# Optimization experiments

Measured on AMD Instinct MI355X. Metric: run time of the kernel, lower is better.

## Reference

```python
import jax, jax.numpy as jnp
import numpy as np

F_SIZE = 256
N_HEAD = 4
D_HEAD = F_SIZE // N_HEAD
B = 16384
E = 31  # number of 'other' entities


def setup_inputs() -> dict:
    key = jax.random.key(0)
    ks = jax.random.split(key, 9)
    s = 1.0 / np.sqrt(F_SIZE)  # ~ nn.Linear init scale
    inp = {
        "ego": jax.random.normal(ks[0], (B, 1, F_SIZE), dtype=jnp.float32),
        "others": jax.random.normal(ks[1], (B, E, F_SIZE), dtype=jnp.float32),
        "mask": jax.random.randint(ks[2], (B, E + 1), 0, 2).astype(bool),
        "Wq": jax.random.uniform(ks[3], (F_SIZE, F_SIZE), jnp.float32, -s, s),
        "Wk": jax.random.uniform(ks[4], (F_SIZE, F_SIZE), jnp.float32, -s, s),
        "Wv": jax.random.uniform(ks[5], (F_SIZE, F_SIZE), jnp.float32, -s, s),
        "Wok": jax.random.uniform(ks[6], (F_SIZE, F_SIZE), jnp.float32, -s, s),
        "Wov": jax.random.uniform(ks[7], (F_SIZE, F_SIZE), jnp.float32, -s, s),
        "Wc": jax.random.uniform(ks[8], (F_SIZE, F_SIZE), jnp.float32, -s, s),
    }
    return inp


def reference(ego, others, mask, Wq, Wk, Wv, Wok, Wov, Wc):
    b = others.shape[0]
    e = others.shape[1]
    # nn.Linear(bias=False): y = x @ W.T
    ego_q = (ego @ Wq.T).reshape(b, 1, N_HEAD, D_HEAD)
    ego_k = (ego @ Wk.T).reshape(b, 1, N_HEAD, D_HEAD)
    ego_v = (ego @ Wv.T).reshape(b, 1, N_HEAD, D_HEAD)
    oth_k = (others @ Wok.T).reshape(b, e, N_HEAD, D_HEAD)
    oth_v = (others @ Wov.T).reshape(b, e, N_HEAD, D_HEAD)
    all_k = jnp.concatenate([ego_k, oth_k], axis=1)  # (b, e+1, h, d)
    all_v = jnp.concatenate([ego_v, oth_v], axis=1)
    # scores: single query per head -> (b, h, 1, e+1)
    scores = jnp.einsum('bqhd,bkhd->bhqk', ego_q, all_k) / np.sqrt(D_HEAD)
    scores = jnp.where(mask[:, None, None, :], jnp.float32(-1e9), scores)
    attn = jax.nn.softmax(scores, axis=-1)
    value = jnp.einsum('bhqk,bkhd->bqhd', attn, all_v).reshape(b, F_SIZE)
    res = ((value @ Wc.T) + ego[:, 0, :]) * 0.5
    return res, attn
```

## Files before the change

### kernel.cpp

```cpp
#include <hip/hip_runtime.h>
#include <hip/hip_bf16.h>

typedef __attribute__((ext_vector_type(8))) short bf16x8;
typedef __attribute__((ext_vector_type(4))) float f32x4;

#define NB 16384
#define NE 31

static __device__ __forceinline__ unsigned short f2b(float f) {
  unsigned int u = __builtin_bit_cast(unsigned int, f);
  return (unsigned short)((u + 0x7fffu + ((u >> 16) & 1u)) >> 16);
}
static __device__ __forceinline__ float b2f(unsigned short h) {
  return __builtin_bit_cast(float, ((unsigned int)h) << 16);
}


__global__ void k0_base(const float* __restrict__ wq, const float* __restrict__ wk,
                        const float* __restrict__ wv, const float* __restrict__ wc,
                        unsigned short* __restrict__ W1, unsigned short* __restrict__ W2) {
  int r = blockIdx.x, k = threadIdx.x;
  if (r < 256) {
    W1[r * 256 + k] = f2b(0.125f * wq[r * 256 + k]);
  } else if (r < 512) {
    W1[r * 256 + k] = f2b(wk[(r - 256) * 256 + k]);
  } else if (r < 768) {
    W1[r * 256 + k] = f2b(wv[(r - 512) * 256 + k]);
  } else {
    int n = r - 768;
    W2[n * 1280 + 1024 + k] = f2b(wc[n * 256 + k]);
  }
}

__global__ void k0_wqo(const float* __restrict__ wq, const float* __restrict__ wok,
                       unsigned short* __restrict__ W1) {
  int m = blockIdx.x;
  int k = threadIdx.x;
  int h = m >> 8, c = m & 255;
  float acc = 0.f;
#pragma unroll 8
  for (int d = 0; d < 64; ++d)
    acc = fmaf(wq[(h * 64 + d) * 256 + k], wok[(h * 64 + d) * 256 + c], acc);
  W1[(768 + m) * 256 + k] = f2b(0.125f * acc);
}

__global__ void k0_g(const float* __restrict__ wov, const float* __restrict__ wc,
                     unsigned short* __restrict__ W2) {
  int n = blockIdx.x;
  int t = threadIdx.x;
#pragma unroll 1
  for (int mi = 0; mi < 4; ++mi) {
    float acc = 0.f;
#pragma unroll 8
    for (int d = 0; d < 64; ++d)
      acc = fmaf(wov[(mi * 64 + d) * 256 + t], wc[n * 256 + mi * 64 + d], acc);
    W2[n * 1280 + mi * 256 + t] = f2b(acc);
  }
}

__global__ __launch_bounds__(256, 2)
void k1b(const float* __restrict__ ego, const unsigned short* __restrict__ W1,
         unsigned short* __restrict__ qkv2) {
  __shared__ __align__(16) unsigned short Al[64 * 256];
  const int tid = threadIdx.x;
  const int bM = blockIdx.x * 64;
#pragma unroll
  for (int it = 0; it < 8; ++it) {
    int c = tid + it * 256;
    int row = c >> 5, k8 = c & 31;
    const float4* g = (const float4*)(ego + (size_t)(bM + row) * 256 + k8 * 8);
    float4 x = g[0], y = g[1];
    float t[8] = {x.x, x.y, x.z, x.w, y.x, y.y, y.z, y.w};
    bf16x8 v;
#pragma unroll
    for (int j = 0; j < 8; ++j) v[j] = (short)f2b(t[j]);
    int byteoff = row * 512 + ((k8 * 16) ^ ((row & 7) << 4));
    *(bf16x8*)((char*)Al + byteoff) = v;
  }
  __syncthreads();
  const int w = tid >> 6, lane = tid & 63, lr = lane & 15, lkg = lane >> 4;
#pragma unroll 1
  for (int cb = 0; cb < 7; ++cb) {
    int bN = w * 448 + cb * 64;
    f32x4 acc[4][4];
#pragma unroll
    for (int mt = 0; mt < 4; ++mt)
#pragma unroll
      for (int nt = 0; nt < 4; ++nt) acc[mt][nt] = (f32x4){0.f, 0.f, 0.f, 0.f};
#pragma unroll
    for (int kk = 0; kk < 8; ++kk) {
      int kidx = kk * 32 + lkg * 8;
      bf16x8 bfr[4];
#pragma unroll
      for (int nt = 0; nt < 4; ++nt)
        bfr[nt] = *(const bf16x8*)(W1 + (size_t)(bN + nt * 16 + lr) * 256 + kidx);
#pragma unroll
      for (int mt = 0; mt < 4; ++mt) {
        int row = mt * 16 + lr;
        int byteoff = row * 512 + ((kidx * 2) ^ ((row & 7) << 4));
        bf16x8 a = *(const bf16x8*)((const char*)Al + byteoff);
#pragma unroll
        for (int nt = 0; nt < 4; ++nt)
          acc[mt][nt] = __builtin_amdgcn_mfma_f32_16x16x32_bf16(a, bfr[nt], acc[mt][nt], 0, 0, 0);
      }
    }
#pragma unroll
    for (int mt = 0; mt < 4; ++mt)
#pragma unroll
      for (int nt = 0; nt < 4; ++nt)
#pragma unroll
        for (int j = 0; j < 4; ++j) {
          int row = bM + mt * 16 + lkg * 4 + j;
          int col = bN + nt * 16 + lr;
          qkv2[(size_t)row * 1792 + col] = f2b(acc[mt][nt][j]);
        }
  }
}

__global__ __launch_bounds__(256, 4)
void ks_attn(const float* __restrict__ others, const int* __restrict__ mask,
             const unsigned short* __restrict__ qkv2,
             unsigned short* __restrict__ u,
             float* __restrict__ attnout) {
  __shared__ __align__(16) unsigned short Xr[32 * 264];
  __shared__ __align__(16) unsigned short Qo_l[1024];
  __shared__ __align__(16) unsigned short qk_l[768];
  __shared__ float sco_l[4][32];
  __shared__ float Pl[4][32];
  const int tid = threadIdx.x;
  const size_t b = blockIdx.x;

  {
    int e = tid >> 3, c = tid & 7;
    if (e < 31) {
      const float4* src = (const float4*)(others) + ((b * 31 + e) * 64 + c * 8);
      float4 f[8];
#pragma unroll
      for (int j = 0; j < 8; ++j) f[j] = src[j];
#pragma unroll
      for (int j = 0; j < 4; ++j) {
        bf16x8 v;
        v[0] = (short)f2b(f[2 * j].x);     v[1] = (short)f2b(f[2 * j].y);
        v[2] = (short)f2b(f[2 * j].z);     v[3] = (short)f2b(f[2 * j].w);
        v[4] = (short)f2b(f[2 * j + 1].x); v[5] = (short)f2b(f[2 * j + 1].y);
        v[6] = (short)f2b(f[2 * j + 1].z); v[7] = (short)f2b(f[2 * j + 1].w);
        *(bf16x8*)(&Xr[e * 264 + c * 32 + j * 8]) = v;
      }
    } else {
      bf16x8 z = (bf16x8){0, 0, 0, 0, 0, 0, 0, 0};
#pragma unroll
      for (int j = 0; j < 4; ++j) *(bf16x8*)(&Xr[31 * 264 + c * 32 + j * 8]) = z;
    }
    if (tid < 224) {
      bf16x8 v = *(const bf16x8*)(qkv2 + b * 1792 + tid * 8);
      if (tid < 96) *(bf16x8*)(&qk_l[tid * 8]) = v;
      else          *(bf16x8*)(&Qo_l[(tid - 96) * 8]) = v;
    }
  }
  __syncthreads();

  const int w = tid >> 6, lane = tid & 63, lr = lane & 15, lkg = lane >> 4;

  if (w < 2) {
    f32x4 acc = (f32x4){0.f, 0.f, 0.f, 0.f};
#pragma unroll
    for (int kk = 0; kk < 8; ++kk) {
      bf16x8 a = *(const bf16x8*)(&Qo_l[(lr & 3) * 256 + kk * 32 + lkg * 8]);
      bf16x8 bb = *(const bf16x8*)(&Xr[(w * 16 + lr) * 264 + kk * 32 + lkg * 8]);
      acc = __builtin_amdgcn_mfma_f32_16x16x32_bf16(a, bb, acc, 0, 0, 0);
    }
    if (lkg == 0) {
      int n = w * 16 + lr;
      if (n < NE) {
#pragma unroll
        for (int j = 0; j < 4; ++j) sco_l[j][1 + n] = acc[j];
      }
    }
  } else if (w == 2) {
    int h = lane >> 4, i = lane & 15;
    const unsigned short* q4 = &qk_l[h * 64 + i * 4];
    const unsigned short* k4p = &qk_l[256 + h * 64 + i * 4];
    float s = 0.f;
#pragma unroll
    for (int j = 0; j < 4; ++j) s += b2f(q4[j]) * b2f(k4p[j]);
#pragma unroll
    for (int off = 1; off < 16; off <<= 1) s += __shfl_xor(s, off, 16);
    if (i == 0) sco_l[h][0] = s;
  }
  __syncthreads();

  {
    int key = lane & 31;
    float s = sco_l[w][key];
    if (mask[b * 32 + key] != 0) s = -1e9f;
    float mx = s;
#pragma unroll
    for (int off = 1; off < 32; off <<= 1) mx = fmaxf(mx, __shfl_xor(mx, off, 32));
    float ex = __expf(s - mx);
    float sm = ex;
#pragma unroll
    for (int off = 1; off < 32; off <<= 1) sm += __shfl_xor(sm, off, 32);
    float p = ex / sm;
    if (lane < 32) {
      Pl[w][key] = p;
      attnout[b * 128 + w * 32 + key] = p;
    }
  }

  {
    float a0 = 0.f, a1 = 0.f, a2 = 0.f, a3 = 0.f;
#pragma unroll
    for (int e = 0; e < NE; ++e) {
      float p = Pl[w][1 + e];
      ushort4 xv = *(const ushort4*)(&Xr[e * 264 + lane * 4]);
      a0 = fmaf(p, b2f(xv.x), a0);
      a1 = fmaf(p, b2f(xv.y), a1);
      a2 = fmaf(p, b2f(xv.z), a2);
      a3 = fmaf(p, b2f(xv.w), a3);
    }
    ushort4 st;
    st.x = f2b(a0); st.y = f2b(a1); st.z = f2b(a2); st.w = f2b(a3);
    *(ushort4*)(u + b * 1280 + w * 256 + lane * 4) = st;
    float p0 = Pl[w][0];
    u[b * 1280 + 1024 + w * 64 + lane] = f2b(p0 * b2f(qk_l[512 + w * 64 + lane]));
  }
}

__global__ __launch_bounds__(256, 2)
void k4_out(const unsigned short* __restrict__ u, const unsigned short* __restrict__ W2,
            const float* __restrict__ ego, float* __restrict__ out) {
  __shared__ __align__(16) unsigned short Au[32 * 256];
  const int tid = threadIdx.x;
  const int bM = blockIdx.x * 32;
  const int w = tid >> 6, lane = tid & 63, lr = lane & 15, lkg = lane >> 4;
  f32x4 acc[2][4];
#pragma unroll
  for (int mt = 0; mt < 2; ++mt)
#pragma unroll
    for (int nt = 0; nt < 4; ++nt) acc[mt][nt] = (f32x4){0.f, 0.f, 0.f, 0.f};
#pragma unroll 1
  for (int kc = 0; kc < 5; ++kc) {
#pragma unroll
    for (int it = 0; it < 4; ++it) {
      int c = tid + it * 256;
      int row = c >> 5, k8 = c & 31;
      bf16x8 v = *(const bf16x8*)(u + (size_t)(bM + row) * 1280 + kc * 256 + k8 * 8);
      int byteoff = row * 512 + ((k8 * 16) ^ ((row & 7) << 4));
      *(bf16x8*)((char*)Au + byteoff) = v;
    }
    __syncthreads();
#pragma unroll
    for (int kk = 0; kk < 8; ++kk) {
      int kidx = kk * 32 + lkg * 8;
      bf16x8 bfr[4];
#pragma unroll
      for (int nt = 0; nt < 4; ++nt)
        bfr[nt] = *(const bf16x8*)(W2 + (size_t)(w * 64 + nt * 16 + lr) * 1280 + kc * 256 + kidx);
#pragma unroll
      for (int mt = 0; mt < 2; ++mt) {
        int row = mt * 16 + lr;
        int byteoff = row * 512 + ((kidx * 2) ^ ((row & 7) << 4));
        bf16x8 a = *(const bf16x8*)((const char*)Au + byteoff);
#pragma unroll
        for (int nt = 0; nt < 4; ++nt)
          acc[mt][nt] = __builtin_amdgcn_mfma_f32_16x16x32_bf16(a, bfr[nt], acc[mt][nt], 0, 0, 0);
      }
    }
    __syncthreads();
  }
#pragma unroll
  for (int mt = 0; mt < 2; ++mt)
#pragma unroll
    for (int nt = 0; nt < 4; ++nt)
#pragma unroll
      for (int j = 0; j < 4; ++j) {
        int row = bM + mt * 16 + lkg * 4 + j;
        int col = w * 64 + nt * 16 + lr;
        out[(size_t)row * 256 + col] = (acc[mt][nt][j] + ego[(size_t)row * 256 + col]) * 0.5f;
      }
}

extern "C" void kernel_launch(void* const* d_in, const int* in_sizes, int n_in,
                              void* d_out, int out_size, void* d_ws, size_t ws_size,
                              hipStream_t stream) {
  const float* ego    = (const float*)d_in[0];
  const float* others = (const float*)d_in[1];
  const int*   mask   = (const int*)d_in[2];
  const float* wq  = (const float*)d_in[3];
  const float* wk  = (const float*)d_in[4];
  const float* wv  = (const float*)d_in[5];
  const float* wok = (const float*)d_in[6];
  const float* wov = (const float*)d_in[7];
  const float* wc  = (const float*)d_in[8];

  unsigned short* W1   = (unsigned short*)d_ws;
  unsigned short* W2   = W1 + 1792 * 256;
  unsigned short* qkv2 = W2 + 256 * 1280;
  unsigned short* u    = qkv2 + (size_t)NB * 1792;

  float* res  = (float*)d_out;
  float* attn = res + (size_t)NB * 256;

  hipLaunchKernelGGL(k0_base, dim3(1024), dim3(256), 0, stream, wq, wk, wv, wc, W1, W2);
  hipLaunchKernelGGL(k0_wqo,  dim3(1024), dim3(256), 0, stream, wq, wok, W1);
  hipLaunchKernelGGL(k0_g,    dim3(256),  dim3(256), 0, stream, wov, wc, W2);
  hipLaunchKernelGGL(k1b,     dim3(256),  dim3(256), 0, stream, ego, W1, qkv2);
  hipLaunchKernelGGL(ks_attn, dim3(NB),   dim3(256), 0, stream, others, mask, qkv2, u, attn);
  hipLaunchKernelGGL(k4_out,  dim3(512),  dim3(256), 0, stream, u, W2, ego, res);
}
```

Baseline: 268.1 us.

## Merge weight-prep kernels, halve k1b tile, swizzle Xr LDS, raise attn occupancy

```diff
diff --git a/kernel.cpp b/kernel.cpp
--- a/kernel.cpp
+++ b/kernel.cpp
@@ -15,57 +15,51 @@
   return __builtin_bit_cast(float, ((unsigned int)h) << 16);
 }
 
-
-__global__ void k0_base(const float* __restrict__ wq, const float* __restrict__ wk,
-                        const float* __restrict__ wv, const float* __restrict__ wc,
-                        unsigned short* __restrict__ W1, unsigned short* __restrict__ W2) {
+__global__ void k0_all(const float* __restrict__ wq, const float* __restrict__ wk,
+                       const float* __restrict__ wv, const float* __restrict__ wok,
+                       const float* __restrict__ wov, const float* __restrict__ wc,
+                       unsigned short* __restrict__ W1, unsigned short* __restrict__ W2) {
   int r = blockIdx.x, k = threadIdx.x;
-  if (r < 256) {
-    W1[r * 256 + k] = f2b(0.125f * wq[r * 256 + k]);
-  } else if (r < 512) {
-    W1[r * 256 + k] = f2b(wk[(r - 256) * 256 + k]);
-  } else if (r < 768) {
-    W1[r * 256 + k] = f2b(wv[(r - 512) * 256 + k]);
-  } else {
-    int n = r - 768;
-    W2[n * 1280 + 1024 + k] = f2b(wc[n * 256 + k]);
-  }
-}
-
-__global__ void k0_wqo(const float* __restrict__ wq, const float* __restrict__ wok,
-                       unsigned short* __restrict__ W1) {
-  int m = blockIdx.x;
-  int k = threadIdx.x;
-  int h = m >> 8, c = m & 255;
-  float acc = 0.f;
-#pragma unroll 8
-  for (int d = 0; d < 64; ++d)
-    acc = fmaf(wq[(h * 64 + d) * 256 + k], wok[(h * 64 + d) * 256 + c], acc);
-  W1[(768 + m) * 256 + k] = f2b(0.125f * acc);
-}
-
-__global__ void k0_g(const float* __restrict__ wov, const float* __restrict__ wc,
-                     unsigned short* __restrict__ W2) {
-  int n = blockIdx.x;
-  int t = threadIdx.x;
-#pragma unroll 1
-  for (int mi = 0; mi < 4; ++mi) {
+  if (r < 1024) {
+    if (r < 256) {
+      W1[r * 256 + k] = f2b(0.125f * wq[r * 256 + k]);
+    } else if (r < 512) {
+      W1[r * 256 + k] = f2b(wk[(r - 256) * 256 + k]);
+    } else if (r < 768) {
+      W1[r * 256 + k] = f2b(wv[(r - 512) * 256 + k]);
+    } else {
+      int n = r - 768;
+      W2[n * 1280 + 1024 + k] = f2b(wc[n * 256 + k]);
+    }
+  } else if (r < 2048) {
+    int m = r - 1024;
+    int h = m >> 8, c = m & 255;
     float acc = 0.f;
 #pragma unroll 8
     for (int d = 0; d < 64; ++d)
-      acc = fmaf(wov[(mi * 64 + d) * 256 + t], wc[n * 256 + mi * 64 + d], acc);
-    W2[n * 1280 + mi * 256 + t] = f2b(acc);
+      acc = fmaf(wq[(h * 64 + d) * 256 + k], wok[(h * 64 + d) * 256 + c], acc);
+    W1[(768 + m) * 256 + k] = f2b(0.125f * acc);
+  } else {
+    int n = r - 2048;
+#pragma unroll 1
+    for (int mi = 0; mi < 4; ++mi) {
+      float acc = 0.f;
+#pragma unroll 8
+      for (int d = 0; d < 64; ++d)
+        acc = fmaf(wov[(mi * 64 + d) * 256 + k], wc[n * 256 + mi * 64 + d], acc);
+      W2[n * 1280 + mi * 256 + k] = f2b(acc);
+    }
   }
 }
 
 __global__ __launch_bounds__(256, 2)
 void k1b(const float* __restrict__ ego, const unsigned short* __restrict__ W1,
          unsigned short* __restrict__ qkv2) {
-  __shared__ __align__(16) unsigned short Al[64 * 256];
+  __shared__ __align__(16) unsigned short Al[32 * 256];
   const int tid = threadIdx.x;
-  const int bM = blockIdx.x * 64;
-#pragma unroll
-  for (int it = 0; it < 8; ++it) {
+  const int bM = blockIdx.x * 32;
+#pragma unroll
+  for (int it = 0; it < 4; ++it) {
     int c = tid + it * 256;
     int row = c >> 5, k8 = c & 31;
     const float4* g = (const float4*)(ego + (size_t)(bM + row) * 256 + k8 * 8);
@@ -82,9 +76,9 @@
 #pragma unroll 1
   for (int cb = 0; cb < 7; ++cb) {
     int bN = w * 448 + cb * 64;
-    f32x4 acc[4][4];
-#pragma unroll
-    for (int mt = 0; mt < 4; ++mt)
+    f32x4 acc[2][4];
+#pragma unroll
+    for (int mt = 0; mt < 2; ++mt)
 #pragma unroll
       for (int nt = 0; nt < 4; ++nt) acc[mt][nt] = (f32x4){0.f, 0.f, 0.f, 0.f};
 #pragma unroll
@@ -95,7 +89,7 @@
       for (int nt = 0; nt < 4; ++nt)
         bfr[nt] = *(const bf16x8*)(W1 + (size_t)(bN + nt * 16 + lr) * 256 + kidx);
 #pragma unroll
-      for (int mt = 0; mt < 4; ++mt) {
+      for (int mt = 0; mt < 2; ++mt) {
         int row = mt * 16 + lr;
         int byteoff = row * 512 + ((kidx * 2) ^ ((row & 7) << 4));
         bf16x8 a = *(const bf16x8*)((const char*)Al + byteoff);
@@ -105,7 +99,7 @@
       }
     }
 #pragma unroll
-    for (int mt = 0; mt < 4; ++mt)
+    for (int mt = 0; mt < 2; ++mt)
 #pragma unroll
       for (int nt = 0; nt < 4; ++nt)
 #pragma unroll
@@ -117,12 +111,12 @@
   }
 }
 
-__global__ __launch_bounds__(256, 4)
+__global__ __launch_bounds__(256, 6)
 void ks_attn(const float* __restrict__ others, const int* __restrict__ mask,
              const unsigned short* __restrict__ qkv2,
              unsigned short* __restrict__ u,
              float* __restrict__ attnout) {
-  __shared__ __align__(16) unsigned short Xr[32 * 264];
+  __shared__ __align__(16) unsigned short Xr[32 * 256];
   __shared__ __align__(16) unsigned short Qo_l[1024];
   __shared__ __align__(16) unsigned short qk_l[768];
   __shared__ float sco_l[4][32];
@@ -134,22 +128,29 @@
     int e = tid >> 3, c = tid & 7;
     if (e < 31) {
       const float4* src = (const float4*)(others) + ((b * 31 + e) * 64 + c * 8);
-      float4 f[8];
-#pragma unroll
-      for (int j = 0; j < 8; ++j) f[j] = src[j];
-#pragma unroll
-      for (int j = 0; j < 4; ++j) {
-        bf16x8 v;
-        v[0] = (short)f2b(f[2 * j].x);     v[1] = (short)f2b(f[2 * j].y);
-        v[2] = (short)f2b(f[2 * j].z);     v[3] = (short)f2b(f[2 * j].w);
-        v[4] = (short)f2b(f[2 * j + 1].x); v[5] = (short)f2b(f[2 * j + 1].y);
-        v[6] = (short)f2b(f[2 * j + 1].z); v[7] = (short)f2b(f[2 * j + 1].w);
-        *(bf16x8*)(&Xr[e * 264 + c * 32 + j * 8]) = v;
+#pragma unroll
+      for (int h = 0; h < 2; ++h) {
+        float4 f[4];
+#pragma unroll
+        for (int j = 0; j < 4; ++j) f[j] = src[h * 4 + j];
+#pragma unroll
+        for (int j = 0; j < 2; ++j) {
+          bf16x8 v;
+          v[0] = (short)f2b(f[2 * j].x);     v[1] = (short)f2b(f[2 * j].y);
+          v[2] = (short)f2b(f[2 * j].z);     v[3] = (short)f2b(f[2 * j].w);
+          v[4] = (short)f2b(f[2 * j + 1].x); v[5] = (short)f2b(f[2 * j + 1].y);
+          v[6] = (short)f2b(f[2 * j + 1].z); v[7] = (short)f2b(f[2 * j + 1].w);
+          int byteoff = e * 512 + ((c * 64 + h * 32 + j * 16) ^ ((e & 7) << 4));
+          *(bf16x8*)((char*)Xr + byteoff) = v;
+        }
       }
     } else {
       bf16x8 z = (bf16x8){0, 0, 0, 0, 0, 0, 0, 0};
 #pragma unroll
-      for (int j = 0; j < 4; ++j) *(bf16x8*)(&Xr[31 * 264 + c * 32 + j * 8]) = z;
+      for (int q4 = 0; q4 < 4; ++q4) {
+        int byteoff = 31 * 512 + ((c * 64 + q4 * 16) ^ ((31 & 7) << 4));
+        *(bf16x8*)((char*)Xr + byteoff) = z;
+      }
     }
     if (tid < 224) {
       bf16x8 v = *(const bf16x8*)(qkv2 + b * 1792 + tid * 8);
@@ -166,7 +167,9 @@
 #pragma unroll
     for (int kk = 0; kk < 8; ++kk) {
       bf16x8 a = *(const bf16x8*)(&Qo_l[(lr & 3) * 256 + kk * 32 + lkg * 8]);
-      bf16x8 bb = *(const bf16x8*)(&Xr[(w * 16 + lr) * 264 + kk * 32 + lkg * 8]);
+      int row = w * 16 + lr;
+      int byteoff = row * 512 + ((kk * 64 + lkg * 16) ^ ((row & 7) << 4));
+      bf16x8 bb = *(const bf16x8*)((const char*)Xr + byteoff);
       acc = __builtin_amdgcn_mfma_f32_16x16x32_bf16(a, bb, acc, 0, 0, 0);
     }
     if (lkg == 0) {
@@ -212,7 +215,8 @@
 #pragma unroll
     for (int e = 0; e < NE; ++e) {
       float p = Pl[w][1 + e];
-      ushort4 xv = *(const ushort4*)(&Xr[e * 264 + lane * 4]);
+      int byteoff = e * 512 + ((lane * 8) ^ ((e & 7) << 4));
+      ushort4 xv = *(const ushort4*)((const char*)Xr + byteoff);
       a0 = fmaf(p, b2f(xv.x), a0);
       a1 = fmaf(p, b2f(xv.y), a1);
       a2 = fmaf(p, b2f(xv.z), a2);
@@ -301,10 +305,9 @@
   float* res  = (float*)d_out;
   float* attn = res + (size_t)NB * 256;
 
-  hipLaunchKernelGGL(k0_base, dim3(1024), dim3(256), 0, stream, wq, wk, wv, wc, W1, W2);
-  hipLaunchKernelGGL(k0_wqo,  dim3(1024), dim3(256), 0, stream, wq, wok, W1);
-  hipLaunchKernelGGL(k0_g,    dim3(256),  dim3(256), 0, stream, wov, wc, W2);
-  hipLaunchKernelGGL(k1b,     dim3(256),  dim3(256), 0, stream, ego, W1, qkv2);
-  hipLaunchKernelGGL(ks_attn, dim3(NB),   dim3(256), 0, stream, others, mask, qkv2, u, attn);
-  hipLaunchKernelGGL(k4_out,  dim3(512),  dim3(256), 0, stream, u, W2, ego, res);
-}
+  hipLaunchKernelGGL(k0_all, dim3(2304), dim3(256), 0, stream,
+                     wq, wk, wv, wok, wov, wc, W1, W2);
+  hipLaunchKernelGGL(k1b,    dim3(512),  dim3(256), 0, stream, ego, W1, qkv2);
+  hipLaunchKernelGGL(ks_attn, dim3(NB),  dim3(256), 0, stream, others, mask, qkv2, u, attn);
+  hipLaunchKernelGGL(k4_out, dim3(512),  dim3(256), 0, stream, u, W2, ego, res);
+}
```

Measured after the change: 302.4 us. +12.8%, slower.
